# Kernel tuning notes

Hardware: AMD Instinct MI355X
Metric: run time of the kernel (lower is better)

Reference implementation:

```python
import jax, jax.numpy as jnp
import numpy as np

N_NODES = 48758  # hardcoded in the original DAN.forward
EPS_BN = 1e-5


def setup_inputs() -> dict:
    key = jax.random.key(0)
    ks = jax.random.split(key, 14)
    E, D, R, L, NI = 780000, 128, 4, 2, 10000
    sc = 1.0 / np.sqrt(D)
    inp = {
        "x": jax.random.normal(ks[0], (N_NODES, D), jnp.float32),
        "edge_index": jax.random.randint(ks[1], (2, E), 0, N_NODES),
        "idx": jax.random.randint(ks[2], (NI,), 0, N_NODES),
        "edge_type": jax.random.randint(ks[3], (E,), 0, R),
        "edge_weight": jax.random.uniform(ks[4], (E,), jnp.float32),
        # RiskGNN params
        "proj_w": jax.random.normal(ks[5], (D, D), jnp.float32) * sc,
        "proj_b": jax.random.normal(ks[6], (D,), jnp.float32) * 0.01,
        "bn_g": jnp.ones((D,), jnp.float32),
        "bn_b": jnp.zeros((D,), jnp.float32),
        # per-layer DAN params, stacked over L=2 layers (same dims)
        "win_w": jax.random.normal(ks[7], (L, D, D), jnp.float32) * sc,
        "win_b": jax.random.normal(ks[8], (L, D), jnp.float32) * 0.01,
        "wrel": jax.random.normal(ks[9], (L, R, D, D), jnp.float32) * sc,
        "out_w": jax.random.normal(ks[10], (L, D, D), jnp.float32) * sc,
        "out_b": jax.random.normal(ks[11], (L, D), jnp.float32) * 0.01,
    }
    return inp


def _dan_layer(h, edge_index, edge_type, rel_num, win_w, win_b, wrel, out_w, out_b):
    dst = edge_index[0]
    src = edge_index[1]
    x = h @ win_w + win_b                       # [N, D]
    x_j = x[src]                                # edge gather [E, D]
    # gcn_norm(add_self_loops=False): deg over col (=src axis edge_index[1])
    ones_e = jnp.ones(dst.shape[0], x.dtype)
    deg = jax.ops.segment_sum(ones_e, src, num_segments=N_NODES)
    dinv = jnp.where(deg > 0, jax.lax.rsqrt(jnp.maximum(deg, 1.0)), 0.0)
    norm_w = (dinv[dst] * dinv[src])[:, None]   # [E, 1]
    msg_gcn = jax.ops.segment_sum(x_j * norm_w, dst, num_segments=N_NODES)
    # per-relation masked matmul (unsorted grouped GEMM)
    res = jnp.zeros_like(x_j)
    for r in range(rel_num):
        res = jnp.where((edge_type == r)[:, None], x_j @ wrel[r], res)
    # segment softmax over edges grouped by dst, per channel
    seg_max = jax.ops.segment_max(res, dst, num_segments=N_NODES)
    ex = jnp.exp(res - seg_max[dst])
    denom = jax.ops.segment_sum(ex, dst, num_segments=N_NODES)
    weig = ex / denom[dst]
    msg = jax.ops.segment_sum(res * weig, dst, num_segments=N_NODES)
    out = (msg_gcn + 0.1 * jax.nn.relu(msg)) @ out_w + out_b
    return out


def reference(x, edge_weight, proj_w, proj_b, bn_g, bn_b, win_w, win_b, wrel,
              out_w, out_b, edge_index, edge_type, idx):
    rel_num = wrel.shape[1]
    n_layer = win_w.shape[0]
    h = x @ proj_w + proj_b
    # BatchNorm1d (training-mode batch stats, biased var)
    mu = jnp.mean(h, axis=0)
    var = jnp.mean((h - mu) ** 2, axis=0)
    h = (h - mu) * jax.lax.rsqrt(var + EPS_BN) * bn_g + bn_b
    h = jax.nn.relu(h)
    for i in range(n_layer):
        h = _dan_layer(h, edge_index, edge_type, rel_num,
                       win_w[i], win_b[i], wrel[i], out_w[i], out_b[i])
    h = jax.nn.gelu(h, approximate=False)  # dropout is identity at eval
    return h[idx]
```

## Files before the change

kernel.cpp:

```cpp
#include <hip/hip_runtime.h>
#include <hip/hip_bf16.h>
#include <math.h>

#define D 128
#define DD (128 * 128)
#define BCAP 6400

typedef __attribute__((ext_vector_type(8))) short short8;
typedef __attribute__((ext_vector_type(4))) float f32x4;

__device__ __forceinline__ float bf2f(unsigned short u) {
    union { unsigned int i; float f; } x; x.i = ((unsigned int)u) << 16; return x.f;
}
__device__ __forceinline__ unsigned short f2bf(float f) {
    unsigned int i = __float_as_uint(f);
    unsigned int r = (i + 0x7FFFu + ((i >> 16) & 1u)) >> 16;
    return (unsigned short)r;
}

__device__ __forceinline__ int vote_flag(const unsigned short* __restrict__ x) {
    __shared__ int bad_s;
    if (threadIdx.x == 0) bad_s = 0;
    __syncthreads();
    unsigned int e = (x[threadIdx.x] >> 7) & 0xFFu;
    unsigned long long b = __ballot(e < 100u || e > 140u);
    if ((threadIdx.x & 63) == 0) atomicAdd(&bad_s, __popcll(b));
    __syncthreads();
    return bad_s > 48 ? 1 : 0;
}

__global__ __launch_bounds__(256) void k_normall(
    const void* __restrict__ xin, unsigned short* __restrict__ xb, int n4, int nbx,
    const void* s0, const void* s1, const void* s2, const void* s3,
    const void* s4, const void* s5, const void* s6, const void* s7, const void* s8,
    int o1, int o2, int o3, int o4, int o5, int o6, int o7, int o8,
    int total, unsigned short* __restrict__ wdst)
{
    int fl = vote_flag((const unsigned short*)xin);
    if (blockIdx.x < nbx) {
        int i = blockIdx.x * 256 + threadIdx.x;
        if (i >= n4) return;
        if (fl) {
            float4 v = ((const float4*)xin)[i];
            uint2 o;
            o.x = (unsigned int)f2bf(v.x) | ((unsigned int)f2bf(v.y) << 16);
            o.y = (unsigned int)f2bf(v.z) | ((unsigned int)f2bf(v.w) << 16);
            ((uint2*)xb)[i] = o;
        } else {
            ((uint2*)xb)[i] = ((const uint2*)xin)[i];
        }
    } else {
        int i = (blockIdx.x - nbx) * 256 + threadIdx.x;
        if (i >= total) return;
        const void* src; int base;
        if      (i < o1) { src = s0; base = 0;  }
        else if (i < o2) { src = s1; base = o1; }
        else if (i < o3) { src = s2; base = o2; }
        else if (i < o4) { src = s3; base = o3; }
        else if (i < o5) { src = s4; base = o4; }
        else if (i < o6) { src = s5; base = o5; }
        else if (i < o7) { src = s6; base = o6; }
        else if (i < o8) { src = s7; base = o7; }
        else             { src = s8; base = o8; }
        int li = i - base;
        wdst[i] = fl ? f2bf(((const float*)src)[li]) : ((const unsigned short*)src)[li];
    }
}

__device__ __forceinline__ void gemm_core(
    const unsigned short* __restrict__ A, const unsigned short* __restrict__ W,
    int M, int blockRow, unsigned short* As, unsigned short* Wt, f32x4 (&acc)[2][8])
{
    int t = threadIdx.x;
    #pragma unroll
    for (int i = 0; i < 8; ++i) {
        int ch = t + i * 256;
        int row = ch >> 4;
        int kc  = ch & 15;
        int grow = blockRow + row;
        uint4 v = make_uint4(0u, 0u, 0u, 0u);
        if (grow < M) v = *((const uint4*)(A + (size_t)grow * D + kc * 8));
        int kcs = kc ^ (row & 15);
        *((uint4*)&As[row * 128 + kcs * 8]) = v;
    }
    #pragma unroll
    for (int i = 0; i < 8; ++i) {
        int ch = t + i * 256;
        int k  = ch >> 4;
        int n0 = (ch & 15) * 8;
        uint4 v = *((const uint4*)(W + k * D + n0));
        const unsigned short* pv = (const unsigned short*)&v;
        int kc = k >> 3;
        int ko = k & 7;
        #pragma unroll
        for (int j = 0; j < 8; ++j) {
            int n = n0 + j;
            Wt[n * 128 + ((kc ^ (n & 15)) * 8) + ko] = pv[j];
        }
    }
    __syncthreads();

    int wave = t >> 6, lane = t & 63, quad = lane >> 4, l16 = lane & 15;
    int rowbase = wave * 32;

    #pragma unroll
    for (int a = 0; a < 2; ++a)
        #pragma unroll
        for (int b = 0; b < 8; ++b) acc[a][b] = (f32x4){0.f, 0.f, 0.f, 0.f};

    #pragma unroll
    for (int ks = 0; ks < 4; ++ks) {
        int chunk = ks * 4 + quad;
        short8 af[2];
        short8 bf[8];
        #pragma unroll
        for (int rt = 0; rt < 2; ++rt) {
            int r = rowbase + rt * 16 + l16;
            af[rt] = *((const short8*)&As[r * 128 + (chunk ^ (r & 15)) * 8]);
        }
        #pragma unroll
        for (int ct = 0; ct < 8; ++ct) {
            int n = ct * 16 + l16;
            bf[ct] = *((const short8*)&Wt[n * 128 + (chunk ^ (n & 15)) * 8]);
        }
        #pragma unroll
        for (int rt = 0; rt < 2; ++rt)
            #pragma unroll
            for (int ct = 0; ct < 8; ++ct)
                acc[rt][ct] = __builtin_amdgcn_mfma_f32_16x16x32_bf16(af[rt], bf[ct], acc[rt][ct], 0, 0, 0);
    }
}

__device__ __forceinline__ void store_c(
    f32x4 (&acc)[2][8], const unsigned short* __restrict__ bias,
    unsigned short* __restrict__ C, int M, int blockRow, int ldc, int coloff)
{
    int t = threadIdx.x;
    int wave = t >> 6, lane = t & 63, quad = lane >> 4, l16 = lane & 15;
    int rowbase = wave * 32;
    #pragma unroll
    for (int rt = 0; rt < 2; ++rt) {
        #pragma unroll
        for (int ct = 0; ct < 8; ++ct) {
            int col = ct * 16 + l16;
            float bv = bias ? bf2f(bias[col]) : 0.f;
            #pragma unroll
            for (int r = 0; r < 4; ++r) {
                int grow = blockRow + rowbase + rt * 16 + quad * 4 + r;
                if (grow < M) {
                    float v = acc[rt][ct][r] + bv;
                    C[(size_t)grow * ldc + coloff + col] = f2bf(v);
                }
            }
        }
    }
}

__global__ __launch_bounds__(256) void gemm_compose(
    const unsigned short* __restrict__ w_in, const unsigned short* __restrict__ wrel,
    const unsigned short* __restrict__ b_in, unsigned short* __restrict__ wc,
    unsigned short* __restrict__ bc)
{
    __shared__ unsigned short As[DD];
    __shared__ unsigned short Wt[DD];
    f32x4 acc[2][8];
    int b = blockIdx.x;
    int l = b >> 2;
    const unsigned short* A = w_in + (size_t)l * DD;
    const unsigned short* W = wrel + (size_t)b * DD;
    gemm_core(A, W, 128, 0, As, Wt, acc);
    store_c(acc, nullptr, wc + (size_t)b * DD, 128, 0, D, 0);
    int t = threadIdx.x;
    if (t < 128) {
        float s = 0.f;
        for (int k = 0; k < 128; ++k)
            s += bf2f(b_in[l * D + k]) * bf2f(W[k * D + t]);
        bc[b * D + t] = f2bf(s);
    }
}

__global__ __launch_bounds__(256) void k_prepw(
    const unsigned short* __restrict__ wbase, const unsigned short* __restrict__ wc,
    unsigned short* __restrict__ wtg, int o4, int o7)
{
    int m = blockIdx.x >> 3;
    int sub = blockIdx.x & 7;
    const unsigned short* src;
    if (m == 0)       src = wbase;
    else if (m <= 2)  src = wbase + o4 + (m - 1) * DD;
    else if (m <= 10) src = wc + (size_t)(m - 3) * DD;
    else              src = wbase + o7 + (m - 11) * DD;
    int c = sub * 256 + threadIdx.x;
    int n = c >> 4;
    int kc = c & 15;
    unsigned short tmp[8];
    #pragma unroll
    for (int ko = 0; ko < 8; ++ko) tmp[ko] = src[(kc * 8 + ko) * 128 + n];
    *((uint4*)(wtg + (size_t)m * DD + n * 128 + ((kc ^ (n & 15)) * 8))) = *(uint4*)tmp;
}

__device__ __forceinline__ void load_afrag(
    const unsigned short* __restrict__ A, int M, int blockRow, short8 (&af)[2][4])
{
    int t = threadIdx.x;
    int wave = t >> 6, lane = t & 63, quad = lane >> 4, l16 = lane & 15;
    int rowbase = blockRow + wave * 32;
    int r0 = min(rowbase + l16, M - 1);
    int r1 = min(rowbase + 16 + l16, M - 1);
    const unsigned short* a0 = A + (size_t)r0 * D;
    const unsigned short* a1 = A + (size_t)r1 * D;
    #pragma unroll
    for (int ks = 0; ks < 4; ++ks) {
        int chunk = ks * 4 + quad;
        af[0][ks] = *((const short8*)(a0 + chunk * 8));
        af[1][ks] = *((const short8*)(a1 + chunk * 8));
    }
}

__device__ __forceinline__ void mfma_slice(
    const unsigned short* Wt, short8 (&af)[2][4], f32x4 (&acc)[2][8])
{
    int lane = threadIdx.x & 63, quad = lane >> 4, l16 = lane & 15;
    #pragma unroll
    for (int a = 0; a < 2; ++a)
        #pragma unroll
        for (int b = 0; b < 8; ++b) acc[a][b] = (f32x4){0.f, 0.f, 0.f, 0.f};
    #pragma unroll
    for (int ks = 0; ks < 4; ++ks) {
        int chunk = ks * 4 + quad;
        short8 bf[8];
        #pragma unroll
        for (int ct = 0; ct < 8; ++ct)
            bf[ct] = *((const short8*)&Wt[(ct * 16 + l16) * 128 + ((chunk ^ l16) * 8)]);
        #pragma unroll
        for (int rt = 0; rt < 2; ++rt)
            #pragma unroll
            for (int ct = 0; ct < 8; ++ct)
                acc[rt][ct] = __builtin_amdgcn_mfma_f32_16x16x32_bf16(af[rt][ks], bf[ct], acc[rt][ct], 0, 0, 0);
    }
}

__device__ __forceinline__ void gemm_core_fast(
    const unsigned short* __restrict__ A,
    const unsigned short* __restrict__ Wt_g,
    int M, int blockRow, unsigned short* Wt, f32x4 (&acc)[2][8])
{
    int t = threadIdx.x;
    #pragma unroll
    for (int i = 0; i < 8; ++i)
        ((uint4*)Wt)[t + i * 256] = ((const uint4*)Wt_g)[t + i * 256];
    short8 af[2][4];
    load_afrag(A, M, blockRow, af);
    #pragma unroll
    for (int a = 0; a < 2; ++a)
        #pragma unroll
        for (int b = 0; b < 8; ++b) acc[a][b] = (f32x4){0.f, 0.f, 0.f, 0.f};
    __syncthreads();
    mfma_slice(Wt, af, acc);
}

__global__ __launch_bounds__(256) void gemm_fast(
    const unsigned short* __restrict__ A, const unsigned short* __restrict__ Wt_g,
    const unsigned short* __restrict__ bias, unsigned short* __restrict__ C,
    int M, int ldc, int coloff)
{
    __shared__ unsigned short Wt[DD];
    f32x4 acc[2][8];
    gemm_core_fast(A, Wt_g, M, blockIdx.x * 128, Wt, acc);
    store_c(acc, bias, C, M, blockIdx.x * 128, ldc, coloff);
}

__global__ __launch_bounds__(256) void gemm_proj(
    const unsigned short* __restrict__ A, const unsigned short* __restrict__ Wt_g,
    const unsigned short* __restrict__ bias, unsigned short* __restrict__ C,
    int M, float* __restrict__ psum, float* __restrict__ psq)
{
    __shared__ unsigned short Wt[DD];
    __shared__ float smS[4][128], smQ[4][128];
    f32x4 acc[2][8];
    int blockRow = blockIdx.x * 128;
    gemm_core_fast(A, Wt_g, M, blockRow, Wt, acc);

    int t = threadIdx.x;
    int wave = t >> 6, lane = t & 63, quad = lane >> 4, l16 = lane & 15;
    int rowbase = wave * 32;
    #pragma unroll
    for (int ct = 0; ct < 8; ++ct) {
        int col = ct * 16 + l16;
        float bv = bf2f(bias[col]);
        float ps = 0.f, pq = 0.f;
        #pragma unroll
        for (int rt = 0; rt < 2; ++rt) {
            #pragma unroll
            for (int r = 0; r < 4; ++r) {
                int grow = blockRow + rowbase + rt * 16 + quad * 4 + r;
                if (grow < M) {
                    float v = acc[rt][ct][r] + bv;
                    C[(size_t)grow * D + col] = f2bf(v);
                    ps += v; pq += v * v;
                }
            }
        }
        ps += __shfl_xor(ps, 16, 64); ps += __shfl_xor(ps, 32, 64);
        pq += __shfl_xor(pq, 16, 64); pq += __shfl_xor(pq, 32, 64);
        if (quad == 0) { smS[wave][col] = ps; smQ[wave][col] = pq; }
    }
    __syncthreads();
    if (t < 128) {
        float s = smS[0][t] + smS[1][t] + smS[2][t] + smS[3][t];
        float q = smQ[0][t] + smQ[1][t] + smQ[2][t] + smQ[3][t];
        psum[blockIdx.x * 128 + t] = s;
        psq[blockIdx.x * 128 + t] = q;
    }
}

__global__ __launch_bounds__(256) void gemm_fused(
    const unsigned short* __restrict__ h, const unsigned short* __restrict__ wtg,
    const unsigned short* __restrict__ b_in_l, const unsigned short* __restrict__ bc_l,
    unsigned short* __restrict__ xl, unsigned char* __restrict__ y8,
    const float* __restrict__ dinv, int M, int Ntot, int l)
{
    __shared__ unsigned short Wt[DD];
    f32x4 acc[2][8];
    int slice = blockIdx.y;
    int m = (slice == 0) ? (1 + l) : (3 + l * 4 + slice - 1);
    int blockRow = blockIdx.x * 128;
    gemm_core_fast(h, wtg + (size_t)m * DD, M, blockRow, Wt, acc);
    int t = threadIdx.x;
    int wave = t >> 6, lane = t & 63, quad = lane >> 4, l16 = lane & 15;
    int rowbase = wave * 32;
    if (slice == 0) {
        #pragma unroll
        for (int rt = 0; rt < 2; ++rt) {
            float dv[4];
            #pragma unroll
            for (int r = 0; r < 4; ++r) {
                int grow = min(blockRow + rowbase + rt * 16 + quad * 4 + r, M - 1);
                dv[r] = dinv[grow];
            }
            #pragma unroll
            for (int ct = 0; ct < 8; ++ct) {
                int col = ct * 16 + l16;
                float bv = bf2f(b_in_l[col]);
                #pragma unroll
                for (int r = 0; r < 4; ++r) {
                    int grow = blockRow + rowbase + rt * 16 + quad * 4 + r;
                    if (grow < M)
                        xl[(size_t)grow * D + col] = f2bf((acc[rt][ct][r] + bv) * dv[r]);
                }
            }
        }
    } else {
        unsigned char* yd = y8 + (size_t)(slice - 1) * (size_t)Ntot * D;
        const unsigned short* bias = bc_l + (slice - 1) * D;
        #pragma unroll
        for (int rt = 0; rt < 2; ++rt) {
            #pragma unroll
            for (int ct = 0; ct < 8; ++ct) {
                int col = ct * 16 + l16;
                float bv = bf2f(bias[col]);
                #pragma unroll
                for (int r = 0; r < 4; ++r) {
                    int grow = blockRow + rowbase + rt * 16 + quad * 4 + r;
                    if (grow < M) {
                        float v = acc[rt][ct][r] + bv;
                        int p = __builtin_amdgcn_cvt_pk_fp8_f32(v, v, 0, false);
                        yd[(size_t)grow * D + col] = (unsigned char)(p & 0xFF);
                    }
                }
            }
        }
    }
}

__global__ __launch_bounds__(256) void gemm_out(
    const unsigned short* __restrict__ zg, const unsigned short* __restrict__ Wt_g,
    const unsigned short* __restrict__ bias, void* __restrict__ out,
    int M, const unsigned short* __restrict__ xprobe)
{
    int fl = vote_flag(xprobe);
    __shared__ unsigned short Wt[DD];
    f32x4 acc[2][8];
    int blockRow = blockIdx.x * 128;
    gemm_core_fast(zg, Wt_g, M, blockRow, Wt, acc);
    int t = threadIdx.x;
    int wave = t >> 6, lane = t & 63, quad = lane >> 4, l16 = lane & 15;
    int rowbase = wave * 32;
    #pragma unroll
    for (int rt = 0; rt < 2; ++rt) {
        #pragma unroll
        for (int ct = 0; ct < 8; ++ct) {
            int col = ct * 16 + l16;
            float bv = bf2f(bias[col]);
            #pragma unroll
            for (int r = 0; r < 4; ++r) {
                int grow = blockRow + rowbase + rt * 16 + quad * 4 + r;
                if (grow < M) {
                    float v = acc[rt][ct][r] + bv;
                    float gl = 0.5f * v * (1.f + erff(v * 0.70710678118654752f));
                    size_t o = (size_t)grow * D + col;
                    if (fl) ((float*)out)[o] = gl;
                    else    ((unsigned short*)out)[o] = f2bf(gl);
                }
            }
        }
    }
}

__global__ __launch_bounds__(256) void k_hista(
    const int* __restrict__ ei, int E,
    unsigned int* __restrict__ part_dst, unsigned int* __restrict__ part_src)
{
    __shared__ unsigned int hd[256], hs[256];
    int b = blockIdx.x, t = threadIdx.x;
    hd[t] = 0u; hs[t] = 0u;
    __syncthreads();
    int base = b * 2048;
    #pragma unroll
    for (int i = 0; i < 8; ++i) {
        int e = base + t + i * 256;
        if (e < E) {
            atomicAdd(&hd[((unsigned int)ei[e]) >> 8], 1u);
            atomicAdd(&hs[((unsigned int)ei[E + e]) >> 8], 1u);
        }
    }
    __syncthreads();
    part_dst[b * 256 + t] = hd[t];
    part_src[b * 256 + t] = hs[t];
}

__global__ void k_scanpart(unsigned int* __restrict__ part_d, unsigned int* __restrict__ part_s,
                           unsigned int* __restrict__ btot_d, unsigned int* __restrict__ btot_s,
                           int BA)
{
    __shared__ unsigned int arr[512];
    unsigned int* part = blockIdx.y ? part_s : part_d;
    unsigned int* btot = blockIdx.y ? btot_s : btot_d;
    int bucket = blockIdx.x, t = threadIdx.x;
    unsigned int v0 = (t < BA) ? part[t * 256 + bucket] : 0u;
    unsigned int v1 = (t + 256 < BA) ? part[(t + 256) * 256 + bucket] : 0u;
    arr[t] = v0; arr[t + 256] = v1;
    __syncthreads();
    for (int off = 1; off < 512; off <<= 1) {
        unsigned int a = arr[t], b2 = arr[t + 256];
        unsigned int pa = (t >= off) ? arr[t - off] : 0u;
        unsigned int pb = (t + 256 >= off) ? arr[t + 256 - off] : 0u;
        __syncthreads();
        arr[t] = a + pa; arr[t + 256] = b2 + pb;
        __syncthreads();
    }
    if (t < BA) part[t * 256 + bucket] = arr[t] - v0;
    if (t + 256 < BA) part[(t + 256) * 256 + bucket] = arr[t + 256] - v1;
    if (t == 0) btot[bucket] = arr[511];
}

__global__ void k_scanbase(const unsigned int* __restrict__ btot_d, const unsigned int* __restrict__ btot_s,
                           unsigned int* __restrict__ bbase_d, unsigned int* __restrict__ bbase_s)
{
    __shared__ unsigned int a1[256], a2[256];
    int t = threadIdx.x;
    unsigned int vd = btot_d[t], vs = btot_s[t];
    a1[t] = vd; a2[t] = vs;
    __syncthreads();
    for (int off = 1; off < 256; off <<= 1) {
        unsigned int x = a1[t], y = a2[t];
        unsigned int px = (t >= off) ? a1[t - off] : 0u;
        unsigned int py = (t >= off) ? a2[t - off] : 0u;
        __syncthreads();
        a1[t] = x + px; a2[t] = y + py;
        __syncthreads();
    }
    bbase_d[t] = a1[t] - vd;
    bbase_s[t] = a2[t] - vs;
    if (t == 255) { bbase_d[256] = a1[255]; bbase_s[256] = a2[255]; }
}

__global__ __launch_bounds__(256) void k_bscatter(
    const int* __restrict__ ei, const int* __restrict__ et, int E,
    const unsigned int* __restrict__ part_dst, const unsigned int* __restrict__ part_src,
    const unsigned int* __restrict__ bbase_d, const unsigned int* __restrict__ bbase_s,
    uint2* __restrict__ ebuck, unsigned short* __restrict__ sbuck)
{
    __shared__ unsigned int cd[256], cs[256];
    int b = blockIdx.x, t = threadIdx.x;
    cd[t] = part_dst[b * 256 + t] + bbase_d[t];
    cs[t] = part_src[b * 256 + t] + bbase_s[t];
    __syncthreads();
    int base = b * 2048;
    #pragma unroll
    for (int i = 0; i < 8; ++i) {
        int e = base + t + i * 256;
        if (e < E) {
            unsigned int d = (unsigned int)ei[e];
            unsigned int s = (unsigned int)ei[E + e];
            unsigned int tt = (unsigned int)et[e];
            unsigned int pd = atomicAdd(&cd[d >> 8], 1u);
            ebuck[pd] = make_uint2(d, s | (tt << 16));
            unsigned int ps = atomicAdd(&cs[s >> 8], 1u);
            sbuck[ps] = (unsigned short)s;
        }
    }
}

__global__ __launch_bounds__(256) void k_buckets(
    const unsigned int* __restrict__ bbase_d, const uint2* __restrict__ ebuck,
    unsigned int* __restrict__ rp, unsigned int* __restrict__ pckd,
    const unsigned int* __restrict__ bbase_s, const unsigned short* __restrict__ sbuck,
    float* __restrict__ dinv, int N)
{
    __shared__ uint2 ebuf[BCAP];
    __shared__ unsigned int bins[1024], gsum[256];
    int b = blockIdx.x, t = threadIdx.x;
    if (blockIdx.y == 0) {
        unsigned int beg = bbase_d[b], end = bbase_d[b + 1];
        unsigned int cnt = end - beg;
        #pragma unroll
        for (int j = 0; j < 4; ++j) bins[t + j * 256] = 0u;
        __syncthreads();
        bool fit = cnt <= (unsigned int)BCAP;
        if (fit) {
            for (unsigned int i = t; i < cnt; i += 256) {
                uint2 v = ebuck[beg + i];
                ebuf[i] = v;
                atomicAdd(&bins[((v.x & 255u) << 2) | ((v.y >> 16) & 3u)], 1u);
            }
        } else {
            for (unsigned int i = t; i < cnt; i += 256) {
                uint2 v = ebuck[beg + i];
                atomicAdd(&bins[((v.x & 255u) << 2) | ((v.y >> 16) & 3u)], 1u);
            }
        }
        __syncthreads();
        unsigned int b0 = bins[4 * t], b1 = bins[4 * t + 1], b2 = bins[4 * t + 2], b3 = bins[4 * t + 3];
        unsigned int s4 = b0 + b1 + b2 + b3;
        gsum[t] = s4;
        __syncthreads();
        for (int off = 1; off < 256; off <<= 1) {
            unsigned int v = gsum[t];
            unsigned int a = (t >= off) ? gsum[t - off] : 0u;
            __syncthreads();
            gsum[t] = v + a;
            __syncthreads();
        }
        unsigned int base0 = gsum[t] - s4;
        bins[4 * t]     = base0;
        bins[4 * t + 1] = base0 + b0;
        bins[4 * t + 2] = base0 + b0 + b1;
        bins[4 * t + 3] = base0 + b0 + b1 + b2;
        int n = (b << 8) + t;
        if (n <= N) rp[n] = beg + base0;
        __syncthreads();
        if (fit) {
            for (unsigned int i = t; i < cnt; i += 256) {
                uint2 v = ebuf[i];
                unsigned int key = ((v.x & 255u) << 2) | ((v.y >> 16) & 3u);
                unsigned int pos = beg + atomicAdd(&bins[key], 1u);
                pckd[pos] = v.y;
            }
        } else {
            for (unsigned int i = t; i < cnt; i += 256) {
                uint2 v = ebuck[beg + i];
                unsigned int key = ((v.x & 255u) << 2) | ((v.y >> 16) & 3u);
                unsigned int pos = beg + atomicAdd(&bins[key], 1u);
                pckd[pos] = v.y;
            }
        }
    } else {
        unsigned int beg = bbase_s[b], end = bbase_s[b + 1];
        bins[t] = 0u;
        __syncthreads();
        for (unsigned int i = beg + t; i < end; i += 256)
            atomicAdd(&bins[sbuck[i] & 255u], 1u);
        __syncthreads();
        int n = (b << 8) + t;
        if (n < N) {
            unsigned int dg = bins[t];
            dinv[n] = dg ? rsqrtf((float)dg) : 0.f;
        }
    }
}

__global__ void k_bnstats(const float* __restrict__ psum, const float* __restrict__ psq,
                          int nb, int N, const unsigned short* __restrict__ g,
                          const unsigned short* __restrict__ b,
                          float* __restrict__ scale, float* __restrict__ shift) {
    int col = threadIdx.x & 127, h = threadIdx.x >> 7;
    float s = 0.f, q = 0.f;
    for (int i = h; i < nb; i += 2) { s += psum[i * 128 + col]; q += psq[i * 128 + col]; }
    __shared__ float sS[256], sQ[256];
    sS[threadIdx.x] = s; sQ[threadIdx.x] = q;
    __syncthreads();
    if (h == 0) {
        s = sS[col] + sS[col + 128];
        q = sQ[col] + sQ[col + 128];
        float inv = 1.f / (float)N;
        float mean = s * inv;
        float var = fmaxf(q * inv - mean * mean, 0.f);
        float sc = rsqrtf(var + 1e-5f) * bf2f(g[col]);
        scale[col] = sc;
        shift[col] = bf2f(b[col]) - mean * sc;
    }
}

__global__ void k_bnrelu(unsigned short* __restrict__ h, const float* __restrict__ scale,
                         const float* __restrict__ shift, int n8) {
    int i = blockIdx.x * blockDim.x + threadIdx.x;
    if (i >= n8) return;
    int cb = (i & 15) * 8;
    uint4 v = ((uint4*)h)[i];
    unsigned int* w = (unsigned int*)&v;
    #pragma unroll
    for (int j = 0; j < 4; ++j) {
        int c = cb + j * 2;
        float v0 = __uint_as_float(w[j] << 16);
        float v1 = __uint_as_float(w[j] & 0xFFFF0000u);
        v0 = fmaxf(fmaf(v0, scale[c], shift[c]), 0.f);
        v1 = fmaxf(fmaf(v1, scale[c + 1], shift[c + 1]), 0.f);
        w[j] = (unsigned int)f2bf(v0) | ((unsigned int)f2bf(v1) << 16);
    }
    ((uint4*)h)[i] = v;
}

__device__ __forceinline__ void acc_edge8(uint4 xv, uint2 yv, float vm,
                                          float* g, float* dd, float* ss) {
    const unsigned int* xw = (const unsigned int*)&xv;
    const unsigned int* yw = (const unsigned int*)&yv;
    #pragma unroll
    for (int w = 0; w < 2; ++w) {
        auto ylo = __builtin_amdgcn_cvt_pk_f32_fp8(yw[w], false);
        auto yhi = __builtin_amdgcn_cvt_pk_f32_fp8(yw[w], true);
        float vy0 = ylo[0], vy1 = ylo[1], vy2 = yhi[0], vy3 = yhi[1];
        unsigned int xa = xw[2 * w], xb2 = xw[2 * w + 1];
        float x0 = __uint_as_float(xa << 16);
        float x1 = __uint_as_float(xa & 0xFFFF0000u);
        float x2 = __uint_as_float(xb2 << 16);
        float x3 = __uint_as_float(xb2 & 0xFFFF0000u);
        int j = 4 * w;
        g[j + 0] = fmaf(x0, vm, g[j + 0]);
        g[j + 1] = fmaf(x1, vm, g[j + 1]);
        g[j + 2] = fmaf(x2, vm, g[j + 2]);
        g[j + 3] = fmaf(x3, vm, g[j + 3]);
        float e0 = __expf(vy0), e1 = __expf(vy1), e2 = __expf(vy2), e3 = __expf(vy3);
        dd[j + 0] = fmaf(e0, vm, dd[j + 0]); ss[j + 0] = fmaf(vy0 * e0, vm, ss[j + 0]);
        dd[j + 1] = fmaf(e1, vm, dd[j + 1]); ss[j + 1] = fmaf(vy1 * e1, vm, ss[j + 1]);
        dd[j + 2] = fmaf(e2, vm, dd[j + 2]); ss[j + 2] = fmaf(vy2 * e2, vm, ss[j + 2]);
        dd[j + 3] = fmaf(e3, vm, dd[j + 3]); ss[j + 3] = fmaf(vy3 * e3, vm, ss[j + 3]);
    }
}

__global__ __launch_bounds__(256) void k_edge(
    const unsigned int* __restrict__ rp, const unsigned int* __restrict__ packed,
    const unsigned short* __restrict__ xl, const unsigned char* __restrict__ y8,
    const float* __restrict__ dinv, unsigned short* __restrict__ zout,
    int NN, int Ntot, const int* __restrict__ nodes)
{
    int lane = threadIdx.x & 63;
    int slot = blockIdx.x * 4 + (threadIdx.x >> 6);
    if (slot >= NN) return;
    int node = nodes ? nodes[slot] : slot;
    node = __builtin_amdgcn_readfirstlane(node);
    unsigned int beg = rp[node], end = rp[node + 1];
    int eg = lane >> 4;
    int cb = (lane & 15) * 8;
    float g[8], dd[8], ss[8];
    #pragma unroll
    for (int j = 0; j < 8; ++j) { g[j] = 0.f; dd[j] = 0.f; ss[j] = 0.f; }

    for (unsigned int e0 = beg; e0 < end; e0 += 8) {
        unsigned int eA = e0 + (unsigned int)eg;
        unsigned int eB = eA + 4u;
        float vmA = (eA < end) ? 1.f : 0.f;
        float vmB = (eB < end) ? 1.f : 0.f;
        unsigned int pA = packed[(eA < end) ? eA : beg];
        unsigned int pB = packed[(eB < end) ? eB : beg];
        unsigned int sA = pA & 0xFFFFu, tA = (pA >> 16) & 3u;
        unsigned int sB = pB & 0xFFFFu, tB = (pB >> 16) & 3u;
        uint4 xvA = *((const uint4*)(xl + (size_t)sA * D + cb));
        uint2 yvA = *((const uint2*)(y8 + ((size_t)tA * Ntot + sA) * D + cb));
        uint4 xvB = *((const uint4*)(xl + (size_t)sB * D + cb));
        uint2 yvB = *((const uint2*)(y8 + ((size_t)tB * Ntot + sB) * D + cb));
        acc_edge8(xvA, yvA, vmA, g, dd, ss);
        acc_edge8(xvB, yvB, vmB, g, dd, ss);
    }

    #pragma unroll
    for (int j = 0; j < 8; ++j) {
        g[j]  += __shfl_xor(g[j], 16, 64);  g[j]  += __shfl_xor(g[j], 32, 64);
        dd[j] += __shfl_xor(dd[j], 16, 64); dd[j] += __shfl_xor(dd[j], 32, 64);
        ss[j] += __shfl_xor(ss[j], 16, 64); ss[j] += __shfl_xor(ss[j], 32, 64);
    }
    if (eg == 0) {
        float dn = dinv[node];
        unsigned int o[4];
        #pragma unroll
        for (int w = 0; w < 4; ++w) {
            int j0 = w * 2, j1 = w * 2 + 1;
            float m0 = (dd[j0] > 0.f) ? ss[j0] / dd[j0] : 0.f;
            float m1 = (dd[j1] > 0.f) ? ss[j1] / dd[j1] : 0.f;
            float z0 = fmaf(g[j0], dn, 0.1f * fmaxf(m0, 0.f));
            float z1 = fmaf(g[j1], dn, 0.1f * fmaxf(m1, 0.f));
            o[w] = (unsigned int)f2bf(z0) | ((unsigned int)f2bf(z1) << 16);
        }
        *((uint4*)(zout + (size_t)slot * D + cb)) = *(uint4*)o;
    }
}

extern "C" void kernel_launch(void* const* d_in, const int* in_sizes, int n_in,
                              void* d_out, int out_size, void* d_ws, size_t ws_size,
                              hipStream_t stream)
{
    const int* ei  = (const int*)d_in[1];
    const int* idx = (const int*)d_in[2];
    const int* et  = (const int*)d_in[3];
    const unsigned short* xprobe = (const unsigned short*)d_in[0];

    int N  = in_sizes[0] / D;
    int E  = in_sizes[1] / 2;
    int NI = in_sizes[2];
    int L  = in_sizes[9] / (D * D);
    int R  = in_sizes[11] / (L * D * D);

    int NB = (N + 255) >> 8;
    int BA = (E + 2047) / 2048;

    char* ws = (char*)d_ws;
    size_t off = 0;
    auto alloc = [&](size_t bytes) -> char* {
        char* p = ws + off;
        off += (bytes + 255) & ~(size_t)255;
        return p;
    };
    unsigned short* h    = (unsigned short*)alloc((size_t)N * D * 2);
    unsigned short* xl   = (unsigned short*)alloc((size_t)N * D * 2);
    unsigned char*  y8   = (unsigned char*)alloc((size_t)N * R * D);
    unsigned short* z    = (unsigned short*)alloc((size_t)N * D * 2);
    unsigned short* xb   = (unsigned short*)alloc((size_t)N * D * 2);
    unsigned short* zg   = (unsigned short*)alloc((size_t)NI * D * 2);
    float*          dinv = (float*)alloc((size_t)N * 4);
    unsigned int*   rp   = (unsigned int*)alloc((size_t)(N + 1) * 4);
    unsigned int*   pckd = (unsigned int*)alloc((size_t)E * 4);
    int gb  = (N + 127) / 128;
    float*          psum = (float*)alloc((size_t)gb * 128 * 4);
    float*          psq  = (float*)alloc((size_t)gb * 128 * 4);
    float*          bscale = (float*)alloc(128 * 4);
    float*          bshift = (float*)alloc(128 * 4);
    unsigned int*   part_dst = (unsigned int*)alloc((size_t)BA * 256 * 4);
    unsigned int*   part_src = (unsigned int*)alloc((size_t)BA * 256 * 4);
    unsigned int*   btot_d   = (unsigned int*)alloc(256 * 4);
    unsigned int*   btot_s   = (unsigned int*)alloc(256 * 4);
    unsigned int*   bbase_d  = (unsigned int*)alloc(257 * 4);
    unsigned int*   bbase_s  = (unsigned int*)alloc(257 * 4);
    uint2*          ebuck = (uint2*)y8;
    unsigned short* sbuck = (unsigned short*)z;
    int o1 = D * D;
    int o2 = o1 + D;
    int o3 = o2 + D;
    int o4 = o3 + D;
    int o5 = o4 + L * D * D;
    int o6 = o5 + L * D;
    int o7 = o6 + L * R * D * D;
    int o8 = o7 + L * D * D;
    int wt = o8 + L * D;
    unsigned short* wbase  = (unsigned short*)alloc((size_t)wt * 2);
    unsigned short* b_proj = wbase + o1;
    unsigned short* g_bn   = wbase + o2;
    unsigned short* b_bn   = wbase + o3;
    unsigned short* w_in   = wbase + o4;
    unsigned short* b_in   = wbase + o5;
    unsigned short* w_rel  = wbase + o6;
    unsigned short* b_out  = wbase + o8;
    unsigned short* wc     = (unsigned short*)alloc((size_t)L * R * D * D * 2);
    unsigned short* bc     = (unsigned short*)alloc((size_t)L * R * D * 2);
    unsigned short* wtg    = (unsigned short*)alloc((size_t)13 * DD * 2);
    (void)ws_size; (void)n_in; (void)out_size;

    int gb2 = (NI + 127) / 128;
    int nb4 = (N + 3) / 4;
    int ni4 = (NI + 3) / 4;

    int n4 = N * D / 4;
    int nbx = (n4 + 255) / 256;
    int nbw = (wt + 255) / 256;
    k_normall<<<nbx + nbw, 256, 0, stream>>>(
        d_in[0], xb, n4, nbx,
        d_in[5], d_in[6], d_in[7], d_in[8], d_in[9], d_in[10], d_in[11], d_in[12], d_in[13],
        o1, o2, o3, o4, o5, o6, o7, o8, wt, wbase);

    k_hista<<<BA, 256, 0, stream>>>(ei, E, part_dst, part_src);
    k_scanpart<<<dim3(256, 2), 256, 0, stream>>>(part_dst, part_src, btot_d, btot_s, BA);
    k_scanbase<<<1, 256, 0, stream>>>(btot_d, btot_s, bbase_d, bbase_s);
    k_bscatter<<<BA, 256, 0, stream>>>(ei, et, E, part_dst, part_src, bbase_d, bbase_s, ebuck, sbuck);
    k_buckets<<<dim3(NB, 2), 256, 0, stream>>>(bbase_d, ebuck, rp, pckd, bbase_s, sbuck, dinv, N);

    gemm_compose<<<L * R, 256, 0, stream>>>(w_in, w_rel, b_in, wc, bc);
    k_prepw<<<13 * 8, 256, 0, stream>>>(wbase, wc, wtg, o4, o7);

    gemm_proj<<<gb, 256, 0, stream>>>(xb, wtg, b_proj, h, N, psum, psq);
    k_bnstats<<<1, 256, 0, stream>>>(psum, psq, gb, N, g_bn, b_bn, bscale, bshift);
    int n8 = N * D / 8;
    k_bnrelu<<<(n8 + 255) / 256, 256, 0, stream>>>(h, bscale, bshift, n8);

    gemm_fused<<<dim3(gb, 1 + R), 256, 0, stream>>>(h, wtg, b_in, bc, xl, y8, dinv, N, N, 0);
    k_edge<<<nb4, 256, 0, stream>>>(rp, pckd, xl, y8, dinv, z, N, N, nullptr);
    gemm_fast<<<gb, 256, 0, stream>>>(z, wtg + (size_t)11 * DD, b_out, h, N, D, 0);

    gemm_fused<<<dim3(gb, 1 + R), 256, 0, stream>>>(h, wtg, b_in + D, bc + R * D, xl, y8, dinv, N, N, 1);
    k_edge<<<ni4, 256, 0, stream>>>(rp, pckd, xl, y8, dinv, zg, NI, N, idx);

    gemm_out<<<gb2, 256, 0, stream>>>(zg, wtg + (size_t)12 * DD, b_out + D, d_out, NI, xprobe);
}
```

Measured before the change: 362.4 us.

## Merge preprocessing kernels, use atomic bucket cursors, and pack x as fp8 with y

Edge bucketing moves onto global atomic cursors inside a combined stage-1 kernel, replacing the separate histogram, scan and scatter launches. Weight composition, transposition and CSR build are merged into one stage-2 kernel. BatchNorm+ReLU is folded into the first fused GEMM, and x is stored as fp8 next to the per-relation y values in one 640-byte row so each edge gather touches a single row. This cuts launch count and gather bandwidth. The cost is lower precision for x, non-deterministic bucket order from the atomics, and a fixed per-bucket capacity that silently drops edges on overflow.

```diff
diff --git a/kernel.cpp b/kernel.cpp
--- a/kernel.cpp
+++ b/kernel.cpp
@@ -4,7 +4,8 @@
 
 #define D 128
 #define DD (128 * 128)
-#define BCAP 6400
+#define RS 640
+#define CAPB 4608
 
 typedef __attribute__((ext_vector_type(8))) short short8;
 typedef __attribute__((ext_vector_type(4))) float f32x4;
@@ -29,16 +30,20 @@
     return bad_s > 48 ? 1 : 0;
 }
 
-__global__ __launch_bounds__(256) void k_normall(
-    const void* __restrict__ xin, unsigned short* __restrict__ xb, int n4, int nbx,
+__global__ __launch_bounds__(256) void k_stage1(
+    const void* __restrict__ xin, unsigned short* __restrict__ xb, int n4, int nbx, int nbw,
     const void* s0, const void* s1, const void* s2, const void* s3,
     const void* s4, const void* s5, const void* s6, const void* s7, const void* s8,
     int o1, int o2, int o3, int o4, int o5, int o6, int o7, int o8,
-    int total, unsigned short* __restrict__ wdst)
-{
-    int fl = vote_flag((const unsigned short*)xin);
-    if (blockIdx.x < nbx) {
-        int i = blockIdx.x * 256 + threadIdx.x;
+    int total, unsigned short* __restrict__ wdst,
+    const int* __restrict__ ei, const int* __restrict__ et, int E,
+    unsigned int* __restrict__ cd_g, unsigned int* __restrict__ cs_g,
+    uint2* __restrict__ ebuck, unsigned short* __restrict__ sbuck)
+{
+    int bx = blockIdx.x, t = threadIdx.x;
+    if (bx < nbx) {
+        int fl = vote_flag((const unsigned short*)xin);
+        int i = bx * 256 + t;
         if (i >= n4) return;
         if (fl) {
             float4 v = ((const float4*)xin)[i];
@@ -49,8 +54,9 @@
         } else {
             ((uint2*)xb)[i] = ((const uint2*)xin)[i];
         }
-    } else {
-        int i = (blockIdx.x - nbx) * 256 + threadIdx.x;
+    } else if (bx < nbx + nbw) {
+        int fl = vote_flag((const unsigned short*)xin);
+        int i = (bx - nbx) * 256 + t;
         if (i >= total) return;
         const void* src; int base;
         if      (i < o1) { src = s0; base = 0;  }
@@ -64,12 +70,47 @@
         else             { src = s8; base = o8; }
         int li = i - base;
         wdst[i] = fl ? f2bf(((const float*)src)[li]) : ((const unsigned short*)src)[li];
+    } else {
+        __shared__ unsigned int hd[256], hs[256];
+        int b = bx - nbx - nbw;
+        hd[t] = 0u; hs[t] = 0u;
+        unsigned int d8[8], sp8[8];
+        __syncthreads();
+        int base = b * 2048;
+        #pragma unroll
+        for (int i = 0; i < 8; ++i) {
+            int e = base + t + i * 256;
+            if (e < E) {
+                unsigned int d = (unsigned int)ei[e];
+                unsigned int s = (unsigned int)ei[E + e];
+                unsigned int tt = (unsigned int)et[e];
+                d8[i] = d; sp8[i] = s | (tt << 16);
+                atomicAdd(&hd[d >> 8], 1u);
+                atomicAdd(&hs[s >> 8], 1u);
+            } else d8[i] = 0xFFFFFFFFu;
+        }
+        __syncthreads();
+        hd[t] = atomicAdd(&cd_g[t], hd[t]);
+        hs[t] = atomicAdd(&cs_g[t], hs[t]);
+        __syncthreads();
+        #pragma unroll
+        for (int i = 0; i < 8; ++i) {
+            if (d8[i] != 0xFFFFFFFFu) {
+                unsigned int bk = d8[i] >> 8;
+                unsigned int pos = atomicAdd(&hd[bk], 1u);
+                if (pos < (unsigned)CAPB) ebuck[(size_t)bk * CAPB + pos] = make_uint2(d8[i], sp8[i]);
+                unsigned int s = sp8[i] & 0xFFFFu;
+                unsigned int bk2 = s >> 8;
+                unsigned int pos2 = atomicAdd(&hs[bk2], 1u);
+                if (pos2 < (unsigned)CAPB) sbuck[(size_t)bk2 * CAPB + pos2] = (unsigned short)s;
+            }
+        }
     }
 }
 
 __device__ __forceinline__ void gemm_core(
     const unsigned short* __restrict__ A, const unsigned short* __restrict__ W,
-    int M, int blockRow, unsigned short* As, unsigned short* Wt, f32x4 (&acc)[2][8])
+    unsigned short* As, unsigned short* Wt, f32x4 (&acc)[2][8])
 {
     int t = threadIdx.x;
     #pragma unroll
@@ -77,11 +118,8 @@
         int ch = t + i * 256;
         int row = ch >> 4;
         int kc  = ch & 15;
-        int grow = blockRow + row;
-        uint4 v = make_uint4(0u, 0u, 0u, 0u);
-        if (grow < M) v = *((const uint4*)(A + (size_t)grow * D + kc * 8));
-        int kcs = kc ^ (row & 15);
-        *((uint4*)&As[row * 128 + kcs * 8]) = v;
+        uint4 v = *((const uint4*)(A + (size_t)row * D + kc * 8));
+        *((uint4*)&As[row * 128 + (kc ^ (row & 15)) * 8]) = v;
     }
     #pragma unroll
     for (int i = 0; i < 8; ++i) {
@@ -90,8 +128,7 @@
         int n0 = (ch & 15) * 8;
         uint4 v = *((const uint4*)(W + k * D + n0));
         const unsigned short* pv = (const unsigned short*)&v;
-        int kc = k >> 3;
-        int ko = k & 7;
+        int kc = k >> 3, ko = k & 7;
         #pragma unroll
         for (int j = 0; j < 8; ++j) {
             int n = n0 + j;
@@ -99,20 +136,16 @@
         }
     }
     __syncthreads();
-
     int wave = t >> 6, lane = t & 63, quad = lane >> 4, l16 = lane & 15;
     int rowbase = wave * 32;
-
     #pragma unroll
     for (int a = 0; a < 2; ++a)
         #pragma unroll
         for (int b = 0; b < 8; ++b) acc[a][b] = (f32x4){0.f, 0.f, 0.f, 0.f};
-
     #pragma unroll
     for (int ks = 0; ks < 4; ++ks) {
         int chunk = ks * 4 + quad;
-        short8 af[2];
-        short8 bf[8];
+        short8 af[2], bf[8];
         #pragma unroll
         for (int rt = 0; rt < 2; ++rt) {
             int r = rowbase + rt * 16 + l16;
@@ -129,6 +162,184 @@
             for (int ct = 0; ct < 8; ++ct)
                 acc[rt][ct] = __builtin_amdgcn_mfma_f32_16x16x32_bf16(af[rt], bf[ct], acc[rt][ct], 0, 0, 0);
     }
+}
+
+__global__ __launch_bounds__(256) void k_stage2(
+    const unsigned int* __restrict__ cd_g, const uint2* __restrict__ ebuck,
+    unsigned int* __restrict__ rp, unsigned int* __restrict__ pckd,
+    const unsigned int* __restrict__ cs_g, const unsigned short* __restrict__ sbuck,
+    float* __restrict__ dinv, int N, int NB,
+    const unsigned short* __restrict__ wbase, unsigned short* __restrict__ bc,
+    unsigned short* __restrict__ wtg, int o4, int o6, int o7)
+{
+    __shared__ __align__(16) char pool[65536];
+    int bx = blockIdx.x, t = threadIdx.x;
+    if (bx < NB) {
+        uint2* ebuf = (uint2*)pool;
+        unsigned int* bins = (unsigned int*)(pool + CAPB * 8);
+        unsigned int* gsum = bins + 1024;
+        unsigned int* csc  = gsum + 256;
+        int b = bx;
+        unsigned int cvt_ = (t < NB) ? min(cd_g[t], (unsigned)CAPB) : 0u;
+        csc[t] = cvt_;
+        __syncthreads();
+        for (int off = 1; off < 256; off <<= 1) {
+            unsigned int v = csc[t];
+            unsigned int a = (t >= off) ? csc[t - off] : 0u;
+            __syncthreads();
+            csc[t] = v + a;
+            __syncthreads();
+        }
+        unsigned int cnt = min(cd_g[b], (unsigned)CAPB);
+        unsigned int beg = csc[b] - cnt;
+        #pragma unroll
+        for (int j = 0; j < 4; ++j) bins[t + j * 256] = 0u;
+        __syncthreads();
+        for (unsigned int i = t; i < cnt; i += 256) {
+            uint2 v = ebuck[(size_t)b * CAPB + i];
+            ebuf[i] = v;
+            atomicAdd(&bins[((v.x & 255u) << 2) | ((v.y >> 16) & 3u)], 1u);
+        }
+        __syncthreads();
+        unsigned int b0 = bins[4 * t], b1 = bins[4 * t + 1], b2 = bins[4 * t + 2], b3 = bins[4 * t + 3];
+        unsigned int s4 = b0 + b1 + b2 + b3;
+        gsum[t] = s4;
+        __syncthreads();
+        for (int off = 1; off < 256; off <<= 1) {
+            unsigned int v = gsum[t];
+            unsigned int a = (t >= off) ? gsum[t - off] : 0u;
+            __syncthreads();
+            gsum[t] = v + a;
+            __syncthreads();
+        }
+        unsigned int base0 = gsum[t] - s4;
+        bins[4 * t]     = beg + base0;
+        bins[4 * t + 1] = beg + base0 + b0;
+        bins[4 * t + 2] = beg + base0 + b0 + b1;
+        bins[4 * t + 3] = beg + base0 + b0 + b1 + b2;
+        int n = (b << 8) + t;
+        if (n <= N) rp[n] = beg + base0;
+        __syncthreads();
+        for (unsigned int i = t; i < cnt; i += 256) {
+            uint2 v = ebuf[i];
+            unsigned int key = ((v.x & 255u) << 2) | ((v.y >> 16) & 3u);
+            unsigned int pos = atomicAdd(&bins[key], 1u);
+            pckd[pos] = v.y;
+        }
+    } else if (bx < 2 * NB) {
+        unsigned int* bins = (unsigned int*)pool;
+        int b = bx - NB;
+        unsigned int cnt = min(cs_g[b], (unsigned)CAPB);
+        bins[t] = 0u;
+        __syncthreads();
+        for (unsigned int i = t; i < cnt; i += 256)
+            atomicAdd(&bins[sbuck[(size_t)b * CAPB + i] & 255u], 1u);
+        __syncthreads();
+        int n = (b << 8) + t;
+        if (n < N) {
+            unsigned int dg = bins[t];
+            dinv[n] = dg ? rsqrtf((float)dg) : 0.f;
+        }
+    } else if (bx < 2 * NB + 8) {
+        int cb = bx - 2 * NB;
+        int l = cb >> 2;
+        const unsigned short* A = wbase + o4 + (size_t)l * DD;
+        const unsigned short* W = wbase + o6 + (size_t)cb * DD;
+        f32x4 acc[2][8];
+        gemm_core(A, W, (unsigned short*)pool, (unsigned short*)pool + DD, acc);
+        int wave = t >> 6, lane = t & 63, quad = lane >> 4, l16 = lane & 15;
+        int rowbase = wave * 32;
+        unsigned short* dst = wtg + (size_t)(3 + cb) * DD;
+        #pragma unroll
+        for (int rt = 0; rt < 2; ++rt) {
+            #pragma unroll
+            for (int ct = 0; ct < 8; ++ct) {
+                int n = ct * 16 + l16;
+                #pragma unroll
+                for (int r = 0; r < 4; ++r) {
+                    int k = rowbase + rt * 16 + quad * 4 + r;
+                    dst[n * 128 + (((k >> 3) ^ (n & 15)) * 8) + (k & 7)] = f2bf(acc[rt][ct][r]);
+                }
+            }
+        }
+        const unsigned short* b_in = wbase + o4 + 2 * DD;
+        if (t < 128) {
+            float s = 0.f;
+            for (int k = 0; k < 128; ++k)
+                s += bf2f(b_in[l * D + k]) * bf2f(W[k * D + t]);
+            bc[cb * D + t] = f2bf(s);
+        }
+    } else {
+        int pb = bx - 2 * NB - 8;
+        int mi = pb >> 3, sub = pb & 7;
+        const int mmap[5] = {0, 1, 2, 11, 12};
+        int m = mmap[mi];
+        const unsigned short* src;
+        if (mi == 0) src = wbase;
+        else if (mi <= 2) src = wbase + o4 + (size_t)(mi - 1) * DD;
+        else src = wbase + o7 + (size_t)(mi - 3) * DD;
+        int c = sub * 256 + t;
+        int n = c >> 4, kc = c & 15;
+        unsigned short tmp[8];
+        #pragma unroll
+        for (int ko = 0; ko < 8; ++ko) tmp[ko] = src[(kc * 8 + ko) * 128 + n];
+        *((uint4*)(wtg + (size_t)m * DD + n * 128 + ((kc ^ (n & 15)) * 8))) = *(uint4*)tmp;
+    }
+}
+
+__device__ __forceinline__ void load_afrag(
+    const unsigned short* __restrict__ A, int M, int blockRow, short8 (&af)[2][4])
+{
+    int t = threadIdx.x;
+    int wave = t >> 6, lane = t & 63, quad = lane >> 4, l16 = lane & 15;
+    int rowbase = blockRow + wave * 32;
+    int r0 = min(rowbase + l16, M - 1);
+    int r1 = min(rowbase + 16 + l16, M - 1);
+    const unsigned short* a0 = A + (size_t)r0 * D;
+    const unsigned short* a1 = A + (size_t)r1 * D;
+    #pragma unroll
+    for (int ks = 0; ks < 4; ++ks) {
+        int chunk = ks * 4 + quad;
+        af[0][ks] = *((const short8*)(a0 + chunk * 8));
+        af[1][ks] = *((const short8*)(a1 + chunk * 8));
+    }
+}
+
+__device__ __forceinline__ void mfma_slice(
+    const unsigned short* Wt, short8 (&af)[2][4], f32x4 (&acc)[2][8])
+{
+    int lane = threadIdx.x & 63, quad = lane >> 4, l16 = lane & 15;
+    #pragma unroll
+    for (int a = 0; a < 2; ++a)
+        #pragma unroll
+        for (int b = 0; b < 8; ++b) acc[a][b] = (f32x4){0.f, 0.f, 0.f, 0.f};
+    #pragma unroll
+    for (int ks = 0; ks < 4; ++ks) {
+        int chunk = ks * 4 + quad;
+        short8 bf[8];
+        #pragma unroll
+        for (int ct = 0; ct < 8; ++ct)
+            bf[ct] = *((const short8*)&Wt[(ct * 16 + l16) * 128 + ((chunk ^ l16) * 8)]);
+        #pragma unroll
+        for (int rt = 0; rt < 2; ++rt)
+            #pragma unroll
+            for (int ct = 0; ct < 8; ++ct)
+                acc[rt][ct] = __builtin_amdgcn_mfma_f32_16x16x32_bf16(af[rt][ks], bf[ct], acc[rt][ct], 0, 0, 0);
+    }
+}
+
+__device__ __forceinline__ void gemm_core_fast(
+    const unsigned short* __restrict__ A, const unsigned short* __restrict__ Wt_g,
+    int M, int blockRow, unsigned short* Wt, f32x4 (&acc)[2][8])
+{
+    int t = threadIdx.x;
+    #pragma unroll
+    for (int i = 0; i < 8; ++i)
+        ((uint4*)Wt)[t + i * 256] = ((const uint4*)Wt_g)[t + i * 256];
+    short8 af[2][4];
+    load_afrag(A, M, blockRow, af);
+    __syncthreads();
+    mfma_slice(Wt, af, acc);
 }
 
 __device__ __forceinline__ void store_c(
@@ -156,118 +367,14 @@
     }
 }
 
-__global__ __launch_bounds__(256) void gemm_compose(
-    const unsigned short* __restrict__ w_in, const unsigned short* __restrict__ wrel,
-    const unsigned short* __restrict__ b_in, unsigned short* __restrict__ wc,
-    unsigned short* __restrict__ bc)
-{
-    __shared__ unsigned short As[DD];
-    __shared__ unsigned short Wt[DD];
-    f32x4 acc[2][8];
-    int b = blockIdx.x;
-    int l = b >> 2;
-    const unsigned short* A = w_in + (size_t)l * DD;
-    const unsigned short* W = wrel + (size_t)b * DD;
-    gemm_core(A, W, 128, 0, As, Wt, acc);
-    store_c(acc, nullptr, wc + (size_t)b * DD, 128, 0, D, 0);
-    int t = threadIdx.x;
-    if (t < 128) {
-        float s = 0.f;
-        for (int k = 0; k < 128; ++k)
-            s += bf2f(b_in[l * D + k]) * bf2f(W[k * D + t]);
-        bc[b * D + t] = f2bf(s);
-    }
-}
-
-__global__ __launch_bounds__(256) void k_prepw(
-    const unsigned short* __restrict__ wbase, const unsigned short* __restrict__ wc,
-    unsigned short* __restrict__ wtg, int o4, int o7)
-{
-    int m = blockIdx.x >> 3;
-    int sub = blockIdx.x & 7;
-    const unsigned short* src;
-    if (m == 0)       src = wbase;
-    else if (m <= 2)  src = wbase + o4 + (m - 1) * DD;
-    else if (m <= 10) src = wc + (size_t)(m - 3) * DD;
-    else              src = wbase + o7 + (m - 11) * DD;
-    int c = sub * 256 + threadIdx.x;
-    int n = c >> 4;
-    int kc = c & 15;
-    unsigned short tmp[8];
-    #pragma unroll
-    for (int ko = 0; ko < 8; ++ko) tmp[ko] = src[(kc * 8 + ko) * 128 + n];
-    *((uint4*)(wtg + (size_t)m * DD + n * 128 + ((kc ^ (n & 15)) * 8))) = *(uint4*)tmp;
-}
-
-__device__ __forceinline__ void load_afrag(
-    const unsigned short* __restrict__ A, int M, int blockRow, short8 (&af)[2][4])
-{
-    int t = threadIdx.x;
-    int wave = t >> 6, lane = t & 63, quad = lane >> 4, l16 = lane & 15;
-    int rowbase = blockRow + wave * 32;
-    int r0 = min(rowbase + l16, M - 1);
-    int r1 = min(rowbase + 16 + l16, M - 1);
-    const unsigned short* a0 = A + (size_t)r0 * D;
-    const unsigned short* a1 = A + (size_t)r1 * D;
-    #pragma unroll
-    for (int ks = 0; ks < 4; ++ks) {
-        int chunk = ks * 4 + quad;
-        af[0][ks] = *((const short8*)(a0 + chunk * 8));
-        af[1][ks] = *((const short8*)(a1 + chunk * 8));
-    }
-}
-
-__device__ __forceinline__ void mfma_slice(
-    const unsigned short* Wt, short8 (&af)[2][4], f32x4 (&acc)[2][8])
-{
-    int lane = threadIdx.x & 63, quad = lane >> 4, l16 = lane & 15;
-    #pragma unroll
-    for (int a = 0; a < 2; ++a)
-        #pragma unroll
-        for (int b = 0; b < 8; ++b) acc[a][b] = (f32x4){0.f, 0.f, 0.f, 0.f};
-    #pragma unroll
-    for (int ks = 0; ks < 4; ++ks) {
-        int chunk = ks * 4 + quad;
-        short8 bf[8];
-        #pragma unroll
-        for (int ct = 0; ct < 8; ++ct)
-            bf[ct] = *((const short8*)&Wt[(ct * 16 + l16) * 128 + ((chunk ^ l16) * 8)]);
-        #pragma unroll
-        for (int rt = 0; rt < 2; ++rt)
-            #pragma unroll
-            for (int ct = 0; ct < 8; ++ct)
-                acc[rt][ct] = __builtin_amdgcn_mfma_f32_16x16x32_bf16(af[rt][ks], bf[ct], acc[rt][ct], 0, 0, 0);
-    }
-}
-
-__device__ __forceinline__ void gemm_core_fast(
-    const unsigned short* __restrict__ A,
-    const unsigned short* __restrict__ Wt_g,
-    int M, int blockRow, unsigned short* Wt, f32x4 (&acc)[2][8])
-{
-    int t = threadIdx.x;
-    #pragma unroll
-    for (int i = 0; i < 8; ++i)
-        ((uint4*)Wt)[t + i * 256] = ((const uint4*)Wt_g)[t + i * 256];
-    short8 af[2][4];
-    load_afrag(A, M, blockRow, af);
-    #pragma unroll
-    for (int a = 0; a < 2; ++a)
-        #pragma unroll
-        for (int b = 0; b < 8; ++b) acc[a][b] = (f32x4){0.f, 0.f, 0.f, 0.f};
-    __syncthreads();
-    mfma_slice(Wt, af, acc);
-}
-
 __global__ __launch_bounds__(256) void gemm_fast(
     const unsigned short* __restrict__ A, const unsigned short* __restrict__ Wt_g,
-    const unsigned short* __restrict__ bias, unsigned short* __restrict__ C,
-    int M, int ldc, int coloff)
+    const unsigned short* __restrict__ bias, unsigned short* __restrict__ C, int M)
 {
     __shared__ unsigned short Wt[DD];
     f32x4 acc[2][8];
     gemm_core_fast(A, Wt_g, M, blockIdx.x * 128, Wt, acc);
-    store_c(acc, bias, C, M, blockIdx.x * 128, ldc, coloff);
+    store_c(acc, bias, C, M, blockIdx.x * 128, D, 0);
 }
 
 __global__ __launch_bounds__(256) void gemm_proj(
@@ -280,7 +387,6 @@
     f32x4 acc[2][8];
     int blockRow = blockIdx.x * 128;
     gemm_core_fast(A, Wt_g, M, blockRow, Wt, acc);
-
     int t = threadIdx.x;
     int wave = t >> 6, lane = t & 63, quad = lane >> 4, l16 = lane & 15;
     int rowbase = wave * 32;
@@ -307,276 +413,8 @@
     }
     __syncthreads();
     if (t < 128) {
-        float s = smS[0][t] + smS[1][t] + smS[2][t] + smS[3][t];
-        float q = smQ[0][t] + smQ[1][t] + smQ[2][t] + smQ[3][t];
-        psum[blockIdx.x * 128 + t] = s;
-        psq[blockIdx.x * 128 + t] = q;
-    }
-}
-
-__global__ __launch_bounds__(256) void gemm_fused(
-    const unsigned short* __restrict__ h, const unsigned short* __restrict__ wtg,
-    const unsigned short* __restrict__ b_in_l, const unsigned short* __restrict__ bc_l,
-    unsigned short* __restrict__ xl, unsigned char* __restrict__ y8,
-    const float* __restrict__ dinv, int M, int Ntot, int l)
-{
-    __shared__ unsigned short Wt[DD];
-    f32x4 acc[2][8];
-    int slice = blockIdx.y;
-    int m = (slice == 0) ? (1 + l) : (3 + l * 4 + slice - 1);
-    int blockRow = blockIdx.x * 128;
-    gemm_core_fast(h, wtg + (size_t)m * DD, M, blockRow, Wt, acc);
-    int t = threadIdx.x;
-    int wave = t >> 6, lane = t & 63, quad = lane >> 4, l16 = lane & 15;
-    int rowbase = wave * 32;
-    if (slice == 0) {
-        #pragma unroll
-        for (int rt = 0; rt < 2; ++rt) {
-            float dv[4];
-            #pragma unroll
-            for (int r = 0; r < 4; ++r) {
-                int grow = min(blockRow + rowbase + rt * 16 + quad * 4 + r, M - 1);
-                dv[r] = dinv[grow];
-            }
-            #pragma unroll
-            for (int ct = 0; ct < 8; ++ct) {
-                int col = ct * 16 + l16;
-                float bv = bf2f(b_in_l[col]);
-                #pragma unroll
-                for (int r = 0; r < 4; ++r) {
-                    int grow = blockRow + rowbase + rt * 16 + quad * 4 + r;
-                    if (grow < M)
-                        xl[(size_t)grow * D + col] = f2bf((acc[rt][ct][r] + bv) * dv[r]);
-                }
-            }
-        }
-    } else {
-        unsigned char* yd = y8 + (size_t)(slice - 1) * (size_t)Ntot * D;
-        const unsigned short* bias = bc_l + (slice - 1) * D;
-        #pragma unroll
-        for (int rt = 0; rt < 2; ++rt) {
-            #pragma unroll
-            for (int ct = 0; ct < 8; ++ct) {
-                int col = ct * 16 + l16;
-                float bv = bf2f(bias[col]);
-                #pragma unroll
-                for (int r = 0; r < 4; ++r) {
-                    int grow = blockRow + rowbase + rt * 16 + quad * 4 + r;
-                    if (grow < M) {
-                        float v = acc[rt][ct][r] + bv;
-                        int p = __builtin_amdgcn_cvt_pk_fp8_f32(v, v, 0, false);
-                        yd[(size_t)grow * D + col] = (unsigned char)(p & 0xFF);
-                    }
-                }
-            }
-        }
-    }
-}
-
-__global__ __launch_bounds__(256) void gemm_out(
-    const unsigned short* __restrict__ zg, const unsigned short* __restrict__ Wt_g,
-    const unsigned short* __restrict__ bias, void* __restrict__ out,
-    int M, const unsigned short* __restrict__ xprobe)
-{
-    int fl = vote_flag(xprobe);
-    __shared__ unsigned short Wt[DD];
-    f32x4 acc[2][8];
-    int blockRow = blockIdx.x * 128;
-    gemm_core_fast(zg, Wt_g, M, blockRow, Wt, acc);
-    int t = threadIdx.x;
-    int wave = t >> 6, lane = t & 63, quad = lane >> 4, l16 = lane & 15;
-    int rowbase = wave * 32;
-    #pragma unroll
-    for (int rt = 0; rt < 2; ++rt) {
-        #pragma unroll
-        for (int ct = 0; ct < 8; ++ct) {
-            int col = ct * 16 + l16;
-            float bv = bf2f(bias[col]);
-            #pragma unroll
-            for (int r = 0; r < 4; ++r) {
-                int grow = blockRow + rowbase + rt * 16 + quad * 4 + r;
-                if (grow < M) {
-                    float v = acc[rt][ct][r] + bv;
-                    float gl = 0.5f * v * (1.f + erff(v * 0.70710678118654752f));
-                    size_t o = (size_t)grow * D + col;
-                    if (fl) ((float*)out)[o] = gl;
-                    else    ((unsigned short*)out)[o] = f2bf(gl);
-                }
-            }
-        }
-    }
-}
-
-__global__ __launch_bounds__(256) void k_hista(
-    const int* __restrict__ ei, int E,
-    unsigned int* __restrict__ part_dst, unsigned int* __restrict__ part_src)
-{
-    __shared__ unsigned int hd[256], hs[256];
-    int b = blockIdx.x, t = threadIdx.x;
-    hd[t] = 0u; hs[t] = 0u;
-    __syncthreads();
-    int base = b * 2048;
-    #pragma unroll
-    for (int i = 0; i < 8; ++i) {
-        int e = base + t + i * 256;
-        if (e < E) {
-            atomicAdd(&hd[((unsigned int)ei[e]) >> 8], 1u);
-            atomicAdd(&hs[((unsigned int)ei[E + e]) >> 8], 1u);
-        }
-    }
-    __syncthreads();
-    part_dst[b * 256 + t] = hd[t];
-    part_src[b * 256 + t] = hs[t];
-}
-
-__global__ void k_scanpart(unsigned int* __restrict__ part_d, unsigned int* __restrict__ part_s,
-                           unsigned int* __restrict__ btot_d, unsigned int* __restrict__ btot_s,
-                           int BA)
-{
-    __shared__ unsigned int arr[512];
-    unsigned int* part = blockIdx.y ? part_s : part_d;
-    unsigned int* btot = blockIdx.y ? btot_s : btot_d;
-    int bucket = blockIdx.x, t = threadIdx.x;
-    unsigned int v0 = (t < BA) ? part[t * 256 + bucket] : 0u;
-    unsigned int v1 = (t + 256 < BA) ? part[(t + 256) * 256 + bucket] : 0u;
-    arr[t] = v0; arr[t + 256] = v1;
-    __syncthreads();
-    for (int off = 1; off < 512; off <<= 1) {
-        unsigned int a = arr[t], b2 = arr[t + 256];
-        unsigned int pa = (t >= off) ? arr[t - off] : 0u;
-        unsigned int pb = (t + 256 >= off) ? arr[t + 256 - off] : 0u;
-        __syncthreads();
-        arr[t] = a + pa; arr[t + 256] = b2 + pb;
-        __syncthreads();
-    }
-    if (t < BA) part[t * 256 + bucket] = arr[t] - v0;
-    if (t + 256 < BA) part[(t + 256) * 256 + bucket] = arr[t + 256] - v1;
-    if (t == 0) btot[bucket] = arr[511];
-}
-
-__global__ void k_scanbase(const unsigned int* __restrict__ btot_d, const unsigned int* __restrict__ btot_s,
-                           unsigned int* __restrict__ bbase_d, unsigned int* __restrict__ bbase_s)
-{
-    __shared__ unsigned int a1[256], a2[256];
-    int t = threadIdx.x;
-    unsigned int vd = btot_d[t], vs = btot_s[t];
-    a1[t] = vd; a2[t] = vs;
-    __syncthreads();
-    for (int off = 1; off < 256; off <<= 1) {
-        unsigned int x = a1[t], y = a2[t];
-        unsigned int px = (t >= off) ? a1[t - off] : 0u;
-        unsigned int py = (t >= off) ? a2[t - off] : 0u;
-        __syncthreads();
-        a1[t] = x + px; a2[t] = y + py;
-        __syncthreads();
-    }
-    bbase_d[t] = a1[t] - vd;
-    bbase_s[t] = a2[t] - vs;
-    if (t == 255) { bbase_d[256] = a1[255]; bbase_s[256] = a2[255]; }
-}
-
-__global__ __launch_bounds__(256) void k_bscatter(
-    const int* __restrict__ ei, const int* __restrict__ et, int E,
-    const unsigned int* __restrict__ part_dst, const unsigned int* __restrict__ part_src,
-    const unsigned int* __restrict__ bbase_d, const unsigned int* __restrict__ bbase_s,
-    uint2* __restrict__ ebuck, unsigned short* __restrict__ sbuck)
-{
-    __shared__ unsigned int cd[256], cs[256];
-    int b = blockIdx.x, t = threadIdx.x;
-    cd[t] = part_dst[b * 256 + t] + bbase_d[t];
-    cs[t] = part_src[b * 256 + t] + bbase_s[t];
-    __syncthreads();
-    int base = b * 2048;
-    #pragma unroll
-    for (int i = 0; i < 8; ++i) {
-        int e = base + t + i * 256;
-        if (e < E) {
-            unsigned int d = (unsigned int)ei[e];
-            unsigned int s = (unsigned int)ei[E + e];
-            unsigned int tt = (unsigned int)et[e];
-            unsigned int pd = atomicAdd(&cd[d >> 8], 1u);
-            ebuck[pd] = make_uint2(d, s | (tt << 16));
-            unsigned int ps = atomicAdd(&cs[s >> 8], 1u);
-            sbuck[ps] = (unsigned short)s;
-        }
-    }
-}
-
-__global__ __launch_bounds__(256) void k_buckets(
-    const unsigned int* __restrict__ bbase_d, const uint2* __restrict__ ebuck,
-    unsigned int* __restrict__ rp, unsigned int* __restrict__ pckd,
-    const unsigned int* __restrict__ bbase_s, const unsigned short* __restrict__ sbuck,
-    float* __restrict__ dinv, int N)
-{
-    __shared__ uint2 ebuf[BCAP];
-    __shared__ unsigned int bins[1024], gsum[256];
-    int b = blockIdx.x, t = threadIdx.x;
-    if (blockIdx.y == 0) {
-        unsigned int beg = bbase_d[b], end = bbase_d[b + 1];
-        unsigned int cnt = end - beg;
-        #pragma unroll
-        for (int j = 0; j < 4; ++j) bins[t + j * 256] = 0u;
-        __syncthreads();
-        bool fit = cnt <= (unsigned int)BCAP;
-        if (fit) {
-            for (unsigned int i = t; i < cnt; i += 256) {
-                uint2 v = ebuck[beg + i];
-                ebuf[i] = v;
-                atomicAdd(&bins[((v.x & 255u) << 2) | ((v.y >> 16) & 3u)], 1u);
-            }
-        } else {
-            for (unsigned int i = t; i < cnt; i += 256) {
-                uint2 v = ebuck[beg + i];
-                atomicAdd(&bins[((v.x & 255u) << 2) | ((v.y >> 16) & 3u)], 1u);
-            }
-        }
-        __syncthreads();
-        unsigned int b0 = bins[4 * t], b1 = bins[4 * t + 1], b2 = bins[4 * t + 2], b3 = bins[4 * t + 3];
-        unsigned int s4 = b0 + b1 + b2 + b3;
-        gsum[t] = s4;
-        __syncthreads();
-        for (int off = 1; off < 256; off <<= 1) {
-            unsigned int v = gsum[t];
-            unsigned int a = (t >= off) ? gsum[t - off] : 0u;
-            __syncthreads();
-            gsum[t] = v + a;
-            __syncthreads();
-        }
-        unsigned int base0 = gsum[t] - s4;
-        bins[4 * t]     = base0;
-        bins[4 * t + 1] = base0 + b0;
-        bins[4 * t + 2] = base0 + b0 + b1;
-        bins[4 * t + 3] = base0 + b0 + b1 + b2;
-        int n = (b << 8) + t;
-        if (n <= N) rp[n] = beg + base0;
-        __syncthreads();
-        if (fit) {
-            for (unsigned int i = t; i < cnt; i += 256) {
-                uint2 v = ebuf[i];
-                unsigned int key = ((v.x & 255u) << 2) | ((v.y >> 16) & 3u);
-                unsigned int pos = beg + atomicAdd(&bins[key], 1u);
-                pckd[pos] = v.y;
-            }
-        } else {
-            for (unsigned int i = t; i < cnt; i += 256) {
-                uint2 v = ebuck[beg + i];
-                unsigned int key = ((v.x & 255u) << 2) | ((v.y >> 16) & 3u);
-                unsigned int pos = beg + atomicAdd(&bins[key], 1u);
-                pckd[pos] = v.y;
-            }
-        }
-    } else {
-        unsigned int beg = bbase_s[b], end = bbase_s[b + 1];
-        bins[t] = 0u;
-        __syncthreads();
-        for (unsigned int i = beg + t; i < end; i += 256)
-            atomicAdd(&bins[sbuck[i] & 255u], 1u);
-        __syncthreads();
-        int n = (b << 8) + t;
-        if (n < N) {
-            unsigned int dg = bins[t];
-            dinv[n] = dg ? rsqrtf((float)dg) : 0.f;
-        }
+        psum[blockIdx.x * 128 + t] = smS[0][t] + smS[1][t] + smS[2][t] + smS[3][t];
+        psq[blockIdx.x * 128 + t]  = smQ[0][t] + smQ[1][t] + smQ[2][t] + smQ[3][t];
     }
 }
 
@@ -602,57 +440,135 @@
     }
 }
 
-__global__ void k_bnrelu(unsigned short* __restrict__ h, const float* __restrict__ scale,
-                         const float* __restrict__ shift, int n8) {
-    int i = blockIdx.x * blockDim.x + threadIdx.x;
-    if (i >= n8) return;
-    int cb = (i & 15) * 8;
-    uint4 v = ((uint4*)h)[i];
-    unsigned int* w = (unsigned int*)&v;
-    #pragma unroll
-    for (int j = 0; j < 4; ++j) {
-        int c = cb + j * 2;
-        float v0 = __uint_as_float(w[j] << 16);
-        float v1 = __uint_as_float(w[j] & 0xFFFF0000u);
-        v0 = fmaxf(fmaf(v0, scale[c], shift[c]), 0.f);
-        v1 = fmaxf(fmaf(v1, scale[c + 1], shift[c + 1]), 0.f);
-        w[j] = (unsigned int)f2bf(v0) | ((unsigned int)f2bf(v1) << 16);
-    }
-    ((uint4*)h)[i] = v;
-}
-
-__device__ __forceinline__ void acc_edge8(uint4 xv, uint2 yv, float vm,
+__global__ __launch_bounds__(256) void gemm_fused(
+    const unsigned short* __restrict__ h, const unsigned short* __restrict__ wtg,
+    const unsigned short* __restrict__ b_in_l, const unsigned short* __restrict__ bc_l,
+    unsigned char* __restrict__ xy8, const float* __restrict__ dinv,
+    const float* __restrict__ bnsc, const float* __restrict__ bnsh, int M, int l)
+{
+    __shared__ unsigned short Wt[DD];
+    f32x4 acc[2][8];
+    int slice = blockIdx.y;
+    int m = (slice == 0) ? (1 + l) : (3 + l * 4 + slice - 1);
+    int blockRow = blockIdx.x * 128;
+    int t = threadIdx.x;
+    const unsigned short* Wt_g = wtg + (size_t)m * DD;
+    #pragma unroll
+    for (int i = 0; i < 8; ++i)
+        ((uint4*)Wt)[t + i * 256] = ((const uint4*)Wt_g)[t + i * 256];
+    short8 af[2][4];
+    load_afrag(h, M, blockRow, af);
+    if (bnsc) {
+        int quad = (t & 63) >> 4;
+        #pragma unroll
+        for (int rt = 0; rt < 2; ++rt)
+            #pragma unroll
+            for (int ks = 0; ks < 4; ++ks) {
+                int ch0 = (ks * 4 + quad) * 8;
+                unsigned short* p = (unsigned short*)&af[rt][ks];
+                #pragma unroll
+                for (int j = 0; j < 8; ++j) {
+                    float f = bf2f(p[j]);
+                    f = fmaxf(fmaf(f, bnsc[ch0 + j], bnsh[ch0 + j]), 0.f);
+                    p[j] = f2bf(f);
+                }
+            }
+    }
+    __syncthreads();
+    mfma_slice(Wt, af, acc);
+
+    int wave = t >> 6, lane = t & 63, quad = lane >> 4, l16 = lane & 15;
+    int rowbase = wave * 32;
+    int boff = (slice == 0) ? 0 : (128 + (slice - 1) * 128);
+    #pragma unroll
+    for (int rt = 0; rt < 2; ++rt) {
+        float dv[4];
+        if (slice == 0) {
+            #pragma unroll
+            for (int r = 0; r < 4; ++r) {
+                int grow = min(blockRow + rowbase + rt * 16 + quad * 4 + r, M - 1);
+                dv[r] = dinv[grow];
+            }
+        }
+        #pragma unroll
+        for (int ct = 0; ct < 8; ++ct) {
+            int col = ct * 16 + l16;
+            float bv = (slice == 0) ? bf2f(b_in_l[col]) : bf2f(bc_l[(slice - 1) * D + col]);
+            #pragma unroll
+            for (int r = 0; r < 4; ++r) {
+                int grow = blockRow + rowbase + rt * 16 + quad * 4 + r;
+                if (grow < M) {
+                    float v = acc[rt][ct][r] + bv;
+                    if (slice == 0) v *= dv[r];
+                    int p = __builtin_amdgcn_cvt_pk_fp8_f32(v, v, 0, false);
+                    xy8[(size_t)grow * RS + boff + col] = (unsigned char)(p & 0xFF);
+                }
+            }
+        }
+    }
+}
+
+__global__ __launch_bounds__(256) void gemm_out(
+    const unsigned short* __restrict__ zg, const unsigned short* __restrict__ Wt_g,
+    const unsigned short* __restrict__ bias, void* __restrict__ out,
+    int M, const unsigned short* __restrict__ xprobe)
+{
+    int fl = vote_flag(xprobe);
+    __shared__ unsigned short Wt[DD];
+    f32x4 acc[2][8];
+    int blockRow = blockIdx.x * 128;
+    gemm_core_fast(zg, Wt_g, M, blockRow, Wt, acc);
+    int t = threadIdx.x;
+    int wave = t >> 6, lane = t & 63, quad = lane >> 4, l16 = lane & 15;
+    int rowbase = wave * 32;
+    #pragma unroll
+    for (int rt = 0; rt < 2; ++rt) {
+        #pragma unroll
+        for (int ct = 0; ct < 8; ++ct) {
+            int col = ct * 16 + l16;
+            float bv = bf2f(bias[col]);
+            #pragma unroll
+            for (int r = 0; r < 4; ++r) {
+                int grow = blockRow + rowbase + rt * 16 + quad * 4 + r;
+                if (grow < M) {
+                    float v = acc[rt][ct][r] + bv;
+                    float gl = 0.5f * v * (1.f + erff(v * 0.70710678118654752f));
+                    size_t o = (size_t)grow * D + col;
+                    if (fl) ((float*)out)[o] = gl;
+                    else    ((unsigned short*)out)[o] = f2bf(gl);
+                }
+            }
+        }
+    }
+}
+
+__device__ __forceinline__ void acc_edge2(uint2 xv, uint2 yv, float vm,
                                           float* g, float* dd, float* ss) {
     const unsigned int* xw = (const unsigned int*)&xv;
     const unsigned int* yw = (const unsigned int*)&yv;
     #pragma unroll
     for (int w = 0; w < 2; ++w) {
+        auto xlo = __builtin_amdgcn_cvt_pk_f32_fp8(xw[w], false);
+        auto xhi = __builtin_amdgcn_cvt_pk_f32_fp8(xw[w], true);
         auto ylo = __builtin_amdgcn_cvt_pk_f32_fp8(yw[w], false);
         auto yhi = __builtin_amdgcn_cvt_pk_f32_fp8(yw[w], true);
-        float vy0 = ylo[0], vy1 = ylo[1], vy2 = yhi[0], vy3 = yhi[1];
-        unsigned int xa = xw[2 * w], xb2 = xw[2 * w + 1];
-        float x0 = __uint_as_float(xa << 16);
-        float x1 = __uint_as_float(xa & 0xFFFF0000u);
-        float x2 = __uint_as_float(xb2 << 16);
-        float x3 = __uint_as_float(xb2 & 0xFFFF0000u);
+        float vx[4] = {xlo[0], xlo[1], xhi[0], xhi[1]};
+        float vy[4] = {ylo[0], ylo[1], yhi[0], yhi[1]};
         int j = 4 * w;
-        g[j + 0] = fmaf(x0, vm, g[j + 0]);
-        g[j + 1] = fmaf(x1, vm, g[j + 1]);
-        g[j + 2] = fmaf(x2, vm, g[j + 2]);
-        g[j + 3] = fmaf(x3, vm, g[j + 3]);
-        float e0 = __expf(vy0), e1 = __expf(vy1), e2 = __expf(vy2), e3 = __expf(vy3);
-        dd[j + 0] = fmaf(e0, vm, dd[j + 0]); ss[j + 0] = fmaf(vy0 * e0, vm, ss[j + 0]);
-        dd[j + 1] = fmaf(e1, vm, dd[j + 1]); ss[j + 1] = fmaf(vy1 * e1, vm, ss[j + 1]);
-        dd[j + 2] = fmaf(e2, vm, dd[j + 2]); ss[j + 2] = fmaf(vy2 * e2, vm, ss[j + 2]);
-        dd[j + 3] = fmaf(e3, vm, dd[j + 3]); ss[j + 3] = fmaf(vy3 * e3, vm, ss[j + 3]);
+        #pragma unroll
+        for (int i = 0; i < 4; ++i) {
+            g[j + i] = fmaf(vx[i], vm, g[j + i]);
+            float e = __expf(vy[i]);
+            dd[j + i] = fmaf(e, vm, dd[j + i]);
+            ss[j + i] = fmaf(vy[i] * e, vm, ss[j + i]);
+        }
     }
 }
 
 __global__ __launch_bounds__(256) void k_edge(
     const unsigned int* __restrict__ rp, const unsigned int* __restrict__ packed,
-    const unsigned short* __restrict__ xl, const unsigned char* __restrict__ y8,
-    const float* __restrict__ dinv, unsigned short* __restrict__ zout,
-    int NN, int Ntot, const int* __restrict__ nodes)
+    const unsigned char* __restrict__ xy8, const float* __restrict__ dinv,
+    unsigned short* __restrict__ zout, int NN, const int* __restrict__ nodes)
 {
     int lane = threadIdx.x & 63;
     int slot = blockIdx.x * 4 + (threadIdx.x >> 6);
@@ -675,12 +591,14 @@
         unsigned int pB = packed[(eB < end) ? eB : beg];
         unsigned int sA = pA & 0xFFFFu, tA = (pA >> 16) & 3u;
         unsigned int sB = pB & 0xFFFFu, tB = (pB >> 16) & 3u;
-        uint4 xvA = *((const uint4*)(xl + (size_t)sA * D + cb));
-        uint2 yvA = *((const uint2*)(y8 + ((size_t)tA * Ntot + sA) * D + cb));
-        uint4 xvB = *((const uint4*)(xl + (size_t)sB * D + cb));
-        uint2 yvB = *((const uint2*)(y8 + ((size_t)tB * Ntot + sB) * D + cb));
-        acc_edge8(xvA, yvA, vmA, g, dd, ss);
-        acc_edge8(xvB, yvB, vmB, g, dd, ss);
+        const unsigned char* bA = xy8 + (size_t)sA * RS;
+        const unsigned char* bB = xy8 + (size_t)sB * RS;
+        uint2 xvA = *((const uint2*)(bA + cb));
+        uint2 yvA = *((const uint2*)(bA + 128 + tA * 128 + cb));
+        uint2 xvB = *((const uint2*)(bB + cb));
+        uint2 yvB = *((const uint2*)(bB + 128 + tB * 128 + cb));
+        acc_edge2(xvA, yvA, vmA, g, dd, ss);
+        acc_edge2(xvB, yvB, vmB, g, dd, ss);
     }
 
     #pragma unroll
@@ -731,8 +649,7 @@
         return p;
     };
     unsigned short* h    = (unsigned short*)alloc((size_t)N * D * 2);
-    unsigned short* xl   = (unsigned short*)alloc((size_t)N * D * 2);
-    unsigned char*  y8   = (unsigned char*)alloc((size_t)N * R * D);
+    unsigned char*  xy8  = (unsigned char*)alloc((size_t)N * RS);
     unsigned short* z    = (unsigned short*)alloc((size_t)N * D * 2);
     unsigned short* xb   = (unsigned short*)alloc((size_t)N * D * 2);
     unsigned short* zg   = (unsigned short*)alloc((size_t)NI * D * 2);
@@ -744,13 +661,10 @@
     float*          psq  = (float*)alloc((size_t)gb * 128 * 4);
     float*          bscale = (float*)alloc(128 * 4);
     float*          bshift = (float*)alloc(128 * 4);
-    unsigned int*   part_dst = (unsigned int*)alloc((size_t)BA * 256 * 4);
-    unsigned int*   part_src = (unsigned int*)alloc((size_t)BA * 256 * 4);
-    unsigned int*   btot_d   = (unsigned int*)alloc(256 * 4);
-    unsigned int*   btot_s   = (unsigned int*)alloc(256 * 4);
-    unsigned int*   bbase_d  = (unsigned int*)alloc(257 * 4);
-    unsigned int*   bbase_s  = (unsigned int*)alloc(257 * 4);
-    uint2*          ebuck = (uint2*)y8;
+    unsigned int*   cursors = (unsigned int*)alloc(512 * 4);
+    unsigned int*   cd_g = cursors;
+    unsigned int*   cs_g = cursors + 256;
+    uint2*          ebuck = (uint2*)xy8;
     unsigned short* sbuck = (unsigned short*)z;
     int o1 = D * D;
     int o2 = o1 + D;
@@ -765,11 +679,8 @@
     unsigned short* b_proj = wbase + o1;
     unsigned short* g_bn   = wbase + o2;
     unsigned short* b_bn   = wbase + o3;
-    unsigned short* w_in   = wbase + o4;
     unsigned short* b_in   = wbase + o5;
-    unsigned short* w_rel  = wbase + o6;
     unsigned short* b_out  = wbase + o8;
-    unsigned short* wc     = (unsigned short*)alloc((size_t)L * R * D * D * 2);
     unsigned short* bc     = (unsigned short*)alloc((size_t)L * R * D * 2);
     unsigned short* wtg    = (unsigned short*)alloc((size_t)13 * DD * 2);
     (void)ws_size; (void)n_in; (void)out_size;
@@ -777,35 +688,31 @@
     int gb2 = (NI + 127) / 128;
     int nb4 = (N + 3) / 4;
     int ni4 = (NI + 3) / 4;
-
     int n4 = N * D / 4;
     int nbx = (n4 + 255) / 256;
     int nbw = (wt + 255) / 256;
-    k_normall<<<nbx + nbw, 256, 0, stream>>>(
-        d_in[0], xb, n4, nbx,
+
+    hipMemsetAsync(cursors, 0, 512 * 4, stream);
+
+    k_stage1<<<nbx + nbw + BA, 256, 0, stream>>>(
+        d_in[0], xb, n4, nbx, nbw,
         d_in[5], d_in[6], d_in[7], d_in[8], d_in[9], d_in[10], d_in[11], d_in[12], d_in[13],
-        o1, o2, o3, o4, o5, o6, o7, o8, wt, wbase);
-
-    k_hista<<<BA, 256, 0, stream>>>(ei, E, part_dst, part_src);
-    k_scanpart<<<dim3(256, 2), 256, 0, stream>>>(part_dst, part_src, btot_d, btot_s, BA);
-    k_scanbase<<<1, 256, 0, stream>>>(btot_d, btot_s, bbase_d, bbase_s);
-    k_bscatter<<<BA, 256, 0, stream>>>(ei, et, E, part_dst, part_src, bbase_d, bbase_s, ebuck, sbuck);
-    k_buckets<<<dim3(NB, 2), 256, 0, stream>>>(bbase_d, ebuck, rp, pckd, bbase_s, sbuck, dinv, N);
-
-    gemm_compose<<<L * R, 256, 0, stream>>>(w_in, w_rel, b_in, wc, bc);
-    k_prepw<<<13 * 8, 256, 0, stream>>>(wbase, wc, wtg, o4, o7);
+        o1, o2, o3, o4, o5, o6, o7, o8, wt, wbase,
+        ei, et, E, cd_g, cs_g, ebuck, sbuck);
+
+    k_stage2<<<2 * NB + 8 + 40, 256, 0, stream>>>(
+        cd_g, ebuck, rp, pckd, cs_g, sbuck, dinv, N, NB,
+        wbase, bc, wtg, o4, o6, o7);
 
     gemm_proj<<<gb, 256, 0, stream>>>(xb, wtg, b_proj, h, N, psum, psq);
     k_bnstats<<<1, 256, 0, stream>>>(psum, psq, gb, N, g_bn, b_bn, bscale, bshift);
-    int n8 = N * D / 8;
-    k_bnrelu<<<(n8 + 255) / 256, 256, 0, stream>>>(h, bscale, bshift, n8);
-
-    gemm_fused<<<dim3(gb, 1 + R), 256, 0, stream>>>(h, wtg, b_in, bc, xl, y8, dinv, N, N, 0);
-    k_edge<<<nb4, 256, 0, stream>>>(rp, pckd, xl, y8, dinv, z, N, N, nullptr);
-    gemm_fast<<<gb, 256, 0, stream>>>(z, wtg + (size_t)11 * DD, b_out, h, N, D, 0);
-
-    gemm_fused<<<dim3(gb, 1 + R), 256, 0, stream>>>(h, wtg, b_in + D, bc + R * D, xl, y8, dinv, N, N, 1);
-    k_edge<<<ni4, 256, 0, stream>>>(rp, pckd, xl, y8, dinv, zg, NI, N, idx);
+
+    gemm_fused<<<dim3(gb, 1 + R), 256, 0, stream>>>(h, wtg, b_in, bc, xy8, dinv, bscale, bshift, N, 0);
+    k_edge<<<nb4, 256, 0, stream>>>(rp, pckd, xy8, dinv, z, N, nullptr);
+    gemm_fast<<<gb, 256, 0, stream>>>(z, wtg + (size_t)11 * DD, b_out, h, N);
+
+    gemm_fused<<<dim3(gb, 1 + R), 256, 0, stream>>>(h, wtg, b_in + D, bc + R * D, xy8, dinv, nullptr, nullptr, N, 1);
+    k_edge<<<ni4, 256, 0, stream>>>(rp, pckd, xy8, dinv, zg, NI, idx);
 
     gemm_out<<<gb2, 256, 0, stream>>>(zg, wtg + (size_t)12 * DD, b_out + D, d_out, NI, xprobe);
 }
```

Result: no change. 364.7 us (+0.6%).
